# Kernel optimization log

Hardware: AMD Instinct MI355X
Metric: run time of the kernel (lower is better)

The kernel has to match this reference:

```python
import jax, jax.numpy as jnp
import numpy as np


def _uniform_directions(key, num_thetas, d):
    # dect.generate_uniform_directions: gaussian columns normalized to unit norm, shape [d, T]
    v = jax.random.normal(key, (d, num_thetas), dtype=jnp.float32)
    return v / jnp.linalg.norm(v, axis=0, keepdims=True)


def _compute_ect(x, v, radius, resolution, scale):
    # x: [N, d], v: [d, T] -> nh: [N, T] projections of points onto directions
    nh = x @ v
    # thresholds: [R, 1, 1]
    lin = jnp.linspace(-radius, radius, resolution, dtype=x.dtype)[:, None, None]
    # scaled sigmoid of (threshold - projection), broadcast to [R, N, T]
    ecc = jax.nn.sigmoid(scale * (lin - nh))
    # Euler characteristic curve: sum over points -> [R, T]
    return ecc.sum(axis=1)


def setup_inputs() -> dict:
    key = jax.random.key(0)
    k1, k2 = jax.random.split(key)
    space1 = jax.random.normal(k1, (384, 128), dtype=jnp.float32)
    space2 = jax.random.normal(k2, (384, 32), dtype=jnp.float32)
    return {"space1": space1, "space2": space2}


def reference(space1, space2):
    n1, d1 = space1.shape
    n2, d2 = space2.shape
    RADIUS = 1.0
    SCALE = 500.0
    # directions generated deterministically (seed 42 in original) per space dims
    v1 = _uniform_directions(jax.random.key(42), n1, d1)
    v2 = _uniform_directions(jax.random.key(42), n2, d2)
    input_ect = _compute_ect(space1, v1, RADIUS, n1, SCALE)   # [n1, n1]
    latent_ect = _compute_ect(space2, v2, RADIUS, n2, SCALE)  # [n2, n2]
    # MSELoss (mean reduction)
    loss = jnp.mean((input_ect - latent_ect) ** 2)
    return loss
```

## Files before the change

kernel.cpp:

```cpp
#include <hip/hip_runtime.h>
#include <stdint.h>

#define TT 384
#define NN 384
#define RR 384
#define D1 128
#define D2 32

#define THETA 0.0352f
#define HALF_SLOTS 191.5f
#define BAND_ITERS 14

__device__ float    g_acc = 0.0f;
__device__ unsigned g_cnt = 0u;

__device__ inline void threefry2x32(uint32_t k0, uint32_t k1,
                                    uint32_t x0, uint32_t x1,
                                    uint32_t& o0, uint32_t& o1) {
    uint32_t ks2 = k0 ^ k1 ^ 0x1BD11BDAu;
    x0 += k0; x1 += k1;
    #define TF_ROUND(r) { x0 += x1; x1 = (x1 << (r)) | (x1 >> (32 - (r))); x1 ^= x0; }
    TF_ROUND(13) TF_ROUND(15) TF_ROUND(26) TF_ROUND(6)
    x0 += k1;  x1 += ks2 + 1u;
    TF_ROUND(17) TF_ROUND(29) TF_ROUND(16) TF_ROUND(24)
    x0 += ks2; x1 += k0 + 2u;
    TF_ROUND(13) TF_ROUND(15) TF_ROUND(26) TF_ROUND(6)
    x0 += k0;  x1 += k1 + 3u;
    TF_ROUND(17) TF_ROUND(29) TF_ROUND(16) TF_ROUND(24)
    x0 += k1;  x1 += ks2 + 4u;
    TF_ROUND(13) TF_ROUND(15) TF_ROUND(26) TF_ROUND(6)
    x0 += ks2; x1 += k0 + 5u;
    #undef TF_ROUND
    o0 = x0; o1 = x1;
}

__device__ inline float erfinv_f32(float x) {
    float w = -log1pf(-x * x);
    float p;
    if (w < 5.0f) {
        w = w - 2.5f;
        p =            2.81022636e-08f;
        p = fmaf(p, w, 3.43273939e-07f);
        p = fmaf(p, w, -3.5233877e-06f);
        p = fmaf(p, w, -4.39150654e-06f);
        p = fmaf(p, w, 0.00021858087f);
        p = fmaf(p, w, -0.00125372503f);
        p = fmaf(p, w, -0.00417768164f);
        p = fmaf(p, w, 0.246640727f);
        p = fmaf(p, w, 1.50140941f);
    } else {
        w = sqrtf(w) - 3.0f;
        p =            -0.000200214257f;
        p = fmaf(p, w, 0.000100950558f);
        p = fmaf(p, w, 0.00134934322f);
        p = fmaf(p, w, -0.00367342844f);
        p = fmaf(p, w, 0.00573950773f);
        p = fmaf(p, w, -0.0076224613f);
        p = fmaf(p, w, 0.00943887047f);
        p = fmaf(p, w, 1.00167406f);
        p = fmaf(p, w, 2.83297682f);
    }
    return p * x;
}

__device__ inline float bits_to_normal(uint32_t bits) {
    uint32_t fb = (bits >> 9) | 0x3F800000u;
    float f = __uint_as_float(fb) - 1.0f;
    float lo = __uint_as_float(0xBF7FFFFFu);
    float u = f * 2.0f + lo;
    u = fmaxf(lo, u);
    return 1.41421356237f * erfinv_f32(u);
}

__device__ inline void scatter_point(float p, float sgn,
                                     float* __restrict__ inc,
                                     float* __restrict__ band) {
    int r1  = (int)ceilf((p + (1.0f + THETA)) * HALF_SLOTS);
    int rlo = (int)ceilf((p + (1.0f - THETA)) * HALF_SLOTS);
    if (r1 <= 0)        atomicAdd(&inc[0], sgn);
    else if (r1 <= 383) atomicAdd(&inc[r1], sgn);
    #pragma unroll
    for (int j = 0; j < BAND_ITERS; ++j) {
        int r = rlo + j;
        if (r >= 0 && r < r1 && r < RR) {
            float lin = -1.0f + 2.0f * (float)r / 383.0f;
            float sig = __builtin_amdgcn_rcpf(1.0f + __expf(500.0f * (p - lin)));
            atomicAdd(&band[r], sgn * sig);
        }
    }
}

__global__ void __launch_bounds__(384) ect_fused(
        const float* __restrict__ x1, const float* __restrict__ x2,
        float* __restrict__ out) {
    int t = blockIdx.x;
    int tid = threadIdx.x;
    int lane = tid & 63;
    int w = tid >> 6;
    __shared__ float v1s[D1];
    __shared__ float v2s[D2];
    __shared__ float inc[RR];
    __shared__ float band[RR];
    __shared__ float red[8];

    float g = 0.0f;
    if (tid < D1 + D2) {
        int i = (tid < D1) ? tid : tid - D1;
        uint32_t flat = (uint32_t)i * TT + (uint32_t)t;
        uint32_t o0, o1;
        threefry2x32(0u, 42u, 0u, flat, o0, o1);
        g = bits_to_normal(o0 ^ o1);
    }
    float sq = g * g;
    #pragma unroll
    for (int off = 32; off > 0; off >>= 1) sq += __shfl_xor(sq, off, 64);
    if (lane == 0) red[w] = sq;
    __syncthreads();
    float nrm1 = sqrtf(red[0] + red[1]);
    float nrm2 = sqrtf(red[2]);
    if (tid < D1)           v1s[tid] = g / nrm1;
    else if (tid < D1 + D2) v2s[tid - D1] = g / nrm2;
    inc[tid] = 0.0f;
    band[tid] = 0.0f;
    __syncthreads();

    const float4* __restrict__ x1v = (const float4*)x1;
    const float4* __restrict__ x2v = (const float4*)x2;
    float4 vf1 = *(const float4*)&v1s[4 * (lane & 31)];
    float4 vf2 = *(const float4*)&v2s[4 * (lane & 7)];

    float p1 = 0.0f, p2 = 0.0f;

    int base1 = (w * 64 + (lane >> 5)) * 32 + (lane & 31);
    #pragma unroll 8
    for (int j = 0; j < 32; ++j) {
        float4 xv = x1v[base1 + 64 * j];
        float s = xv.x * vf1.x;
        s = fmaf(xv.y, vf1.y, s);
        s = fmaf(xv.z, vf1.z, s);
        s = fmaf(xv.w, vf1.w, s);
        #pragma unroll
        for (int m = 16; m > 0; m >>= 1) s += __shfl_xor(s, m, 64);
        if ((lane & 31) == j) p1 = s;
    }

    int base2 = (w * 64 + (lane >> 3)) * 8 + (lane & 7);
    #pragma unroll
    for (int j = 0; j < 8; ++j) {
        float4 xv = x2v[base2 + 64 * j];
        float s = xv.x * vf2.x;
        s = fmaf(xv.y, vf2.y, s);
        s = fmaf(xv.z, vf2.z, s);
        s = fmaf(xv.w, vf2.w, s);
        #pragma unroll
        for (int m = 4; m > 0; m >>= 1) s += __shfl_xor(s, m, 64);
        if ((lane & 7) == j) p2 = s;
    }

    scatter_point(p1,  1.0f, inc, band);
    scatter_point(p2, -1.0f, inc, band);
    __syncthreads();

    float v = inc[tid];
    #pragma unroll
    for (int s = 1; s < 64; s <<= 1) {
        float u = __shfl_up(v, s, 64);
        if (lane >= s) v += u;
    }
    if (lane == 63) red[w] = v;
    __syncthreads();
    float off_acc = 0.0f;
    for (int j = 0; j < w; ++j) off_acc += red[j];
    v += off_acc;

    float d = v + band[tid];
    float s2 = d * d;
    #pragma unroll
    for (int off = 32; off > 0; off >>= 1) s2 += __shfl_xor(s2, off, 64);
    __syncthreads();
    if (lane == 0) red[w] = s2;
    __syncthreads();

    if (tid == 0) {
        float s = red[0] + red[1] + red[2] + red[3] + red[4] + red[5];
        atomicAdd(&g_acc, s);
        __threadfence();
        unsigned old = atomicInc(&g_cnt, TT - 1);
        if (old == TT - 1) {
            __threadfence();
            float total = __hip_atomic_load(&g_acc, __ATOMIC_RELAXED,
                                            __HIP_MEMORY_SCOPE_AGENT);
            out[0] = total * (1.0f / ((float)RR * (float)TT));
            __hip_atomic_store(&g_acc, 0.0f, __ATOMIC_RELAXED,
                               __HIP_MEMORY_SCOPE_AGENT);
        }
    }
}

extern "C" void kernel_launch(void* const* d_in, const int* in_sizes, int n_in,
                              void* d_out, int out_size, void* d_ws, size_t ws_size,
                              hipStream_t stream) {
    const float* space1 = (const float*)d_in[0];
    const float* space2 = (const float*)d_in[1];
    float* out = (float*)d_out;

    (void)d_ws; (void)ws_size;

    ect_fused<<<TT, 384, 0, stream>>>(space1, space2, out);
}
```

Baseline: 85.44 us.

## Replace shuffle-reduction dot products with swizzled LDS transpose reduction

```diff
diff --git a/kernel.cpp b/kernel.cpp
--- a/kernel.cpp
+++ b/kernel.cpp
@@ -11,8 +11,8 @@
 #define HALF_SLOTS 191.5f
 #define BAND_ITERS 14
 
-__device__ float    g_acc = 0.0f;
-__device__ unsigned g_cnt = 0u;
+__device__ __attribute__((aligned(256))) float    g_acc = 0.0f;
+__device__ __attribute__((aligned(256))) unsigned g_cnt = 0u;
 
 __device__ inline void threefry2x32(uint32_t k0, uint32_t k1,
                                     uint32_t x0, uint32_t x1,
@@ -102,6 +102,10 @@
     __shared__ float inc[RR];
     __shared__ float band[RR];
     __shared__ float red[8];
+    __shared__ float part1[6][32][64];
+    __shared__ float part2[6][8][64];
+    float* p1f = &part1[0][0][0];
+    float* p2f = &part2[0][0][0];
 
     float g = 0.0f;
     if (tid < D1 + D2) {
@@ -129,9 +133,8 @@
     float4 vf1 = *(const float4*)&v1s[4 * (lane & 31)];
     float4 vf2 = *(const float4*)&v2s[4 * (lane & 7)];
 
-    float p1 = 0.0f, p2 = 0.0f;
-
     int base1 = (w * 64 + (lane >> 5)) * 32 + (lane & 31);
+    int wb1 = w * 32 * 64;
     #pragma unroll 8
     for (int j = 0; j < 32; ++j) {
         float4 xv = x1v[base1 + 64 * j];
@@ -139,12 +142,22 @@
         s = fmaf(xv.y, vf1.y, s);
         s = fmaf(xv.z, vf1.z, s);
         s = fmaf(xv.w, vf1.w, s);
+        p1f[((wb1 + j * 64 + lane) ^ ((j & 7) << 2))] = s;
+    }
+    float4 a4 = {0.0f, 0.0f, 0.0f, 0.0f};
+    {
+        int rb = wb1 + (lane >> 1) * 64 + (lane & 1) * 32;
+        int q  = ((lane >> 1) & 7) << 2;
         #pragma unroll
-        for (int m = 16; m > 0; m >>= 1) s += __shfl_xor(s, m, 64);
-        if ((lane & 31) == j) p1 = s;
-    }
+        for (int i2 = 0; i2 < 8; ++i2) {
+            float4 c = *(const float4*)&p1f[(rb + i2 * 4) ^ q];
+            a4.x += c.x; a4.y += c.y; a4.z += c.z; a4.w += c.w;
+        }
+    }
+    float p1 = (a4.x + a4.y) + (a4.z + a4.w);
 
     int base2 = (w * 64 + (lane >> 3)) * 8 + (lane & 7);
+    int wb2 = w * 8 * 64;
     #pragma unroll
     for (int j = 0; j < 8; ++j) {
         float4 xv = x2v[base2 + 64 * j];
@@ -152,10 +165,19 @@
         s = fmaf(xv.y, vf2.y, s);
         s = fmaf(xv.z, vf2.z, s);
         s = fmaf(xv.w, vf2.w, s);
+        p2f[((wb2 + j * 64 + lane) ^ ((j & 3) << 3))] = s;
+    }
+    float4 b4 = {0.0f, 0.0f, 0.0f, 0.0f};
+    {
+        int rb = wb2 + (lane >> 3) * 64 + (lane & 7) * 8;
+        int q  = ((lane >> 3) & 3) << 3;
         #pragma unroll
-        for (int m = 4; m > 0; m >>= 1) s += __shfl_xor(s, m, 64);
-        if ((lane & 7) == j) p2 = s;
-    }
+        for (int i2 = 0; i2 < 2; ++i2) {
+            float4 c = *(const float4*)&p2f[(rb + i2 * 4) ^ q];
+            b4.x += c.x; b4.y += c.y; b4.z += c.z; b4.w += c.w;
+        }
+    }
+    float p2 = (b4.x + b4.y) + (b4.z + b4.w);
 
     scatter_point(p1,  1.0f, inc, band);
     scatter_point(p2, -1.0f, inc, band);
@@ -183,15 +205,17 @@
 
     if (tid == 0) {
         float s = red[0] + red[1] + red[2] + red[3] + red[4] + red[5];
-        atomicAdd(&g_acc, s);
-        __threadfence();
-        unsigned old = atomicInc(&g_cnt, TT - 1);
+        __hip_atomic_fetch_add(&g_acc, s, __ATOMIC_RELEASE,
+                               __HIP_MEMORY_SCOPE_AGENT);
+        unsigned old = __hip_atomic_fetch_add(&g_cnt, 1u, __ATOMIC_ACQ_REL,
+                                              __HIP_MEMORY_SCOPE_AGENT);
         if (old == TT - 1) {
-            __threadfence();
-            float total = __hip_atomic_load(&g_acc, __ATOMIC_RELAXED,
+            float total = __hip_atomic_load(&g_acc, __ATOMIC_ACQUIRE,
                                             __HIP_MEMORY_SCOPE_AGENT);
             out[0] = total * (1.0f / ((float)RR * (float)TT));
             __hip_atomic_store(&g_acc, 0.0f, __ATOMIC_RELAXED,
+                               __HIP_MEMORY_SCOPE_AGENT);
+            __hip_atomic_store(&g_cnt, 0u, __ATOMIC_RELAXED,
                                __HIP_MEMORY_SCOPE_AGENT);
         }
     }
```

Result: slower. 89.06 us (+4.2%).
